# Optimization experiments

Measured on AMD Instinct MI355X. Metric: run time of the kernel, lower is better.

The kernel has to match this reference:

```python
import jax, jax.numpy as jnp
import numpy as np

N_NODES = 50000
N_EDGES = 800000
D_FEAT = 96


def setup_inputs() -> dict:
    key = jax.random.key(0)
    kx, ks, kd = jax.random.split(key, 3)
    x = jax.random.normal(kx, (N_NODES, D_FEAT), dtype=jnp.float32)
    src = jax.random.randint(ks, (N_EDGES,), 0, N_NODES, dtype=jnp.int64)
    dst = jax.random.randint(kd, (N_EDGES,), 0, N_NODES, dtype=jnp.int64)
    return {"x": x, "src": src, "dst": dst}


def reference(x, src, dst):
    n = x.shape[0]
    ones = jnp.ones(src.shape[0], dtype=x.dtype)
    # out-degree: edges leaving each node (src side)
    out_deg = jnp.clip(jax.ops.segment_sum(ones, src, num_segments=n), 1.0, None)
    # in-degree: edges arriving at each node (dst side)
    in_deg = jnp.clip(jax.ops.segment_sum(ones, dst, num_segments=n), 1.0, None)
    # pre-scale by out-degree^{-1/2}
    xs = x * (out_deg ** -0.5)[:, None]
    # copy_u + sum aggregation: sum messages from src into dst
    agg = jax.ops.segment_sum(xs[src], dst, num_segments=n)
    # post-scale by in-degree^{-1/2}
    return agg * (in_deg ** -0.5)[:, None]
```

## Files before the change

### kernel.cpp

```cpp
#include <hip/hip_runtime.h>


#define D_FEAT 96
#define CAP 64
#define PART_SHIFT 8
#define PNODES 256
#define NP_MAX 256
#define EPB 3072
#define OVF_CAP 8192

__device__ __forceinline__ unsigned short f2bf_rne(float f) {
    unsigned u = __float_as_uint(f);
    unsigned r = (u >> 16) & 1u;
    u += 0x7fffu + r;
    return (unsigned short)(u >> 16);
}


__global__ __launch_bounds__(256) void partition_kernel(
        const int* __restrict__ src, const int* __restrict__ dst,
        int n_edges, int np, int stride,
        int* __restrict__ pcur_d, int* __restrict__ pcur_s,
        unsigned* __restrict__ pbuf_d, unsigned short* __restrict__ pbuf_s,
        int* __restrict__ ctr,
        int* __restrict__ povf_d, int* __restrict__ sovf_d) {
    __shared__ int hcd[NP_MAX], hcs[NP_MAX];
    __shared__ int bd[NP_MAX], bs_[NP_MAX];
    __shared__ int od[NP_MAX], os_[NP_MAX];
    const int base = blockIdx.x * EPB;

    for (int i = threadIdx.x; i < NP_MAX; i += 256) {
        hcd[i] = 0; hcs[i] = 0; od[i] = 0; os_[i] = 0;
    }
    __syncthreads();

    unsigned v[12];
    #pragma unroll
    for (int k = 0; k < 12; ++k) {
        int i = base + (int)threadIdx.x + (k << 8);
        if (i < n_edges) {
            int s = src[i], d = dst[i];
            unsigned pv = (unsigned)d | ((unsigned)s << 16);
            v[k] = pv;
            atomicAdd(&hcd[d >> PART_SHIFT], 1);
            atomicAdd(&hcs[s >> PART_SHIFT], 1);
        }
    }
    __syncthreads();

    for (int p = threadIdx.x; p < np; p += 256) {
        int cd = hcd[p];
        bd[p] = cd ? atomicAdd(&pcur_d[p], cd) : 0;
        int cs = hcs[p];
        bs_[p] = cs ? atomicAdd(&pcur_s[p], cs) : 0;
    }
    __syncthreads();

    #pragma unroll
    for (int k = 0; k < 12; ++k) {
        int i = base + (int)threadIdx.x + (k << 8);
        if (i < n_edges) {
            unsigned pv = v[k];
            int d = (int)(pv & 0xffffu);
            int s = (int)(pv >> 16);
            int pd = d >> PART_SHIFT;
            int j = bd[pd] + atomicAdd(&od[pd], 1);
            if (j < stride) pbuf_d[(size_t)pd * stride + j] = pv;
            else { int k2 = atomicAdd(&ctr[1], 1); if (k2 < OVF_CAP) povf_d[k2] = (int)pv; }
            int ps = s >> PART_SHIFT;
            int j2 = bs_[ps] + atomicAdd(&os_[ps], 1);
            if (j2 < stride) pbuf_s[(size_t)ps * stride + j2] = (unsigned short)s;
            else { int k3 = atomicAdd(&ctr[2], 1); if (k3 < OVF_CAP) sovf_d[k3] = s; }
        }
    }
}


__global__ __launch_bounds__(256) void bincnt_kernel(
        const unsigned* __restrict__ pbuf_d, const int* __restrict__ pcur_d,
        const unsigned short* __restrict__ pbuf_s, const int* __restrict__ pcur_s,
        int stride, int n_nodes,
        const float* __restrict__ x, unsigned* __restrict__ xs,
        int* __restrict__ cursor, int* __restrict__ out_cnt,
        unsigned short* __restrict__ slots,
        int* __restrict__ ctr, int* __restrict__ ovf_d) {
    __shared__ unsigned short lslots[PNODES * CAP];
    __shared__ int lcnt[PNODES];
    __shared__ int lout[PNODES];
    const int b = blockIdx.x;
    const int nbase = b << PART_SHIFT;
    const int nloc = min(PNODES, n_nodes - nbase);

    for (int i = threadIdx.x; i < PNODES; i += 256) { lcnt[i] = 0; lout[i] = 0; }
    __syncthreads();

    int n = pcur_d[b]; if (n > stride) n = stride;
    for (int i = threadIdx.x; i < n; i += 256) {
        unsigned pv = pbuf_d[(size_t)b * stride + i];
        int dl = (int)(pv & 0xffu);
        int s  = (int)(pv >> 16);
        int pos = atomicAdd(&lcnt[dl], 1);
        if (pos < CAP) lslots[dl * CAP + pos] = (unsigned short)s;
        else { int k = atomicAdd(&ctr[0], 1); if (k < OVF_CAP) ovf_d[k] = (int)pv; }
    }
    int n2 = pcur_s[b]; if (n2 > stride) n2 = stride;
    for (int i = threadIdx.x; i < n2; i += 256) {
        int s = (int)pbuf_s[(size_t)b * stride + i];
        atomicAdd(&lout[s & (PNODES - 1)], 1);
    }
    __syncthreads();

    for (int i = threadIdx.x; i < nloc; i += 256) {
        cursor[nbase + i]  = lcnt[i];
        out_cnt[nbase + i] = lout[i];
    }
    const unsigned* ls = (const unsigned*)lslots;
    unsigned* gs = (unsigned*)slots + (size_t)nbase * (CAP / 2);
    const int ncopy = nloc * (CAP / 2);
    for (int i = threadIdx.x; i < ncopy; i += 256) gs[i] = ls[i];

    const int ntot = nloc * 48;
    for (int i = threadIdx.x; i < ntot; i += 256) {
        int nd = i / 48;
        int j  = i - nd * 48;
        int c  = lout[nd];
        float w = rsqrtf((float)(c < 1 ? 1 : c));
        float2 vv = *(const float2*)(x + (size_t)(nbase + nd) * D_FEAT + j * 2);
        unsigned lo = f2bf_rne(vv.x * w);
        unsigned hi = f2bf_rne(vv.y * w);
        xs[(size_t)(nbase + nd) * 48 + j] = lo | (hi << 16);
    }
}

__global__ void fixup_kernel(int* __restrict__ ctr,
                             const int* __restrict__ povf_d,
                             const int* __restrict__ sovf_d,
                             int* __restrict__ ovf_d,
                             int* __restrict__ cursor,
                             int* __restrict__ out_cnt,
                             const float* __restrict__ x,
                             unsigned* __restrict__ xs) {
    int np_ = ctr[1]; if (np_ > OVF_CAP) np_ = OVF_CAP;
    for (int i = threadIdx.x; i < np_; i += 256) {
        unsigned pv = (unsigned)povf_d[i];
        atomicAdd(&cursor[pv & 0xffffu], 1);
        int k = atomicAdd(&ctr[0], 1);
        if (k < OVF_CAP) ovf_d[k] = (int)pv;
    }
    int ns_ = ctr[2]; if (ns_ > OVF_CAP) ns_ = OVF_CAP;
    for (int i = threadIdx.x; i < ns_; i += 256)
        atomicAdd(&out_cnt[(unsigned)sovf_d[i]], 1);
    __syncthreads();
    int total = ns_ * 48;
    for (int i = threadIdx.x; i < total; i += 256) {
        int k = i / 48, j = i - k * 48;
        int s = sovf_d[k];
        int c = out_cnt[s];
        float w = rsqrtf((float)(c < 1 ? 1 : c));
        float2 vv = *(const float2*)(x + (size_t)s * D_FEAT + j * 2);
        unsigned lo = f2bf_rne(vv.x * w);
        unsigned hi = f2bf_rne(vv.y * w);
        xs[(size_t)s * 48 + j] = lo | (hi << 16);
    }
}


__global__ __launch_bounds__(256) void gather_kernel(
        const unsigned* __restrict__ xs,
        const unsigned short* __restrict__ slots,
        const int* __restrict__ cursor,
        const float* __restrict__ x,
        const int* __restrict__ out_cnt,
        const int* __restrict__ ctr,
        const int* __restrict__ ovf_d,
        float* __restrict__ out, int n_nodes) {
    int wid  = threadIdx.x >> 6;
    int lane = threadIdx.x & 63;
    int node = __builtin_amdgcn_readfirstlane(blockIdx.x * 4 + wid);
    if (node >= n_nodes) return;

    int cnt_all = __builtin_amdgcn_readfirstlane(cursor[node]);
    int cnt = cnt_all < CAP ? cnt_all : CAP;

    float accx = 0.f, accy = 0.f;
    const bool act = lane < 48;

    if (cnt > 0) {
        int idx  = lane < cnt ? lane : cnt - 1;
        int sval = (int)slots[node * CAP + idx];

        int e = 0;
        for (; e + 16 <= cnt; e += 16) {
            if (act) {
                unsigned u[16];
                #pragma unroll
                for (int k = 0; k < 16; ++k) {
                    int s = __builtin_amdgcn_readlane(sval, e + k);
                    u[k] = xs[s * 48 + lane];
                }
                #pragma unroll
                for (int k = 0; k < 16; ++k) {
                    accx += __uint_as_float(u[k] << 16);
                    accy += __uint_as_float(u[k] & 0xffff0000u);
                }
            }
        }
        for (; e + 4 <= cnt; e += 4) {
            if (act) {
                unsigned u[4];
                #pragma unroll
                for (int k = 0; k < 4; ++k) {
                    int s = __builtin_amdgcn_readlane(sval, e + k);
                    u[k] = xs[s * 48 + lane];
                }
                #pragma unroll
                for (int k = 0; k < 4; ++k) {
                    accx += __uint_as_float(u[k] << 16);
                    accy += __uint_as_float(u[k] & 0xffff0000u);
                }
            }
        }
        for (; e < cnt; ++e) {
            if (act) {
                int s = __builtin_amdgcn_readlane(sval, e);
                unsigned u0 = xs[s * 48 + lane];
                accx += __uint_as_float(u0 << 16);
                accy += __uint_as_float(u0 & 0xffff0000u);
            }
        }
    }

    if (cnt_all > CAP) {
        int novf = __builtin_amdgcn_readfirstlane(ctr[0]);
        if (novf > OVF_CAP) novf = OVF_CAP;
        for (int k = 0; k < novf; ++k) {
            unsigned pv = (unsigned)ovf_d[k];
            if ((int)(pv & 0xffffu) == node) {
                int s = (int)(pv >> 16);
                int c = out_cnt[s];
                float w = rsqrtf((float)(c < 1 ? 1 : c));
                if (act) {
                    accx += w * x[(size_t)s * D_FEAT + lane * 2];
                    accy += w * x[(size_t)s * D_FEAT + lane * 2 + 1];
                }
            }
        }
    }

    float sc = rsqrtf((float)(cnt_all < 1 ? 1 : cnt_all));
    if (act) {
        float* op = out + (size_t)node * D_FEAT + lane * 2;
        op[0] = accx * sc;
        op[1] = accy * sc;
    }
}


__global__ void degree_kernel(const int* __restrict__ src,
                              const int* __restrict__ dst,
                              int* __restrict__ out_cnt,
                              int* __restrict__ in_cnt, int n_edges) {
    int i = blockIdx.x * blockDim.x + threadIdx.x;
    if (i < n_edges) {
        atomicAdd(&out_cnt[src[i]], 1);
        atomicAdd(&in_cnt[dst[i]], 1);
    }
}

__global__ void scale_kernel(float* __restrict__ osc, float* __restrict__ isc, int n) {
    int i = blockIdx.x * blockDim.x + threadIdx.x;
    if (i < n) {
        int c0 = ((const int*)osc)[i];
        int c1 = ((const int*)isc)[i];
        osc[i] = rsqrtf((float)(c0 < 1 ? 1 : c0));
        isc[i] = rsqrtf((float)(c1 < 1 ? 1 : c1));
    }
}

__global__ void scatter_kernel(const float* __restrict__ x,
                               const int* __restrict__ src,
                               const int* __restrict__ dst,
                               const float* __restrict__ osc,
                               const float* __restrict__ isc,
                               float* __restrict__ out, int n_edges) {
    int idx = blockIdx.x * blockDim.x + threadIdx.x;
    int e = idx / 24, c = idx % 24;
    if (e >= n_edges) return;
    int s = src[e], d = dst[e];
    float w = osc[s] * isc[d];
    const float4 v = *(const float4*)(x + (size_t)s * D_FEAT + c * 4);
    float* o = out + (size_t)d * D_FEAT + c * 4;
    unsafeAtomicAdd(o + 0, v.x * w);
    unsafeAtomicAdd(o + 1, v.y * w);
    unsafeAtomicAdd(o + 2, v.z * w);
    unsafeAtomicAdd(o + 3, v.w * w);
}


extern "C" void kernel_launch(void* const* d_in, const int* in_sizes, int n_in,
                              void* d_out, int out_size, void* d_ws, size_t ws_size,
                              hipStream_t stream) {
    const float* x  = (const float*)d_in[0];
    const int* src  = (const int*)d_in[1];
    const int* dst  = (const int*)d_in[2];
    float* out      = (float*)d_out;

    const int n_edges = in_sizes[1];
    const int n_nodes = in_sizes[0] / D_FEAT;

    const int np = (n_nodes + PNODES - 1) / PNODES;
    const int avg = n_edges / (np > 0 ? np : 1);
    const int stride = avg + avg / 4 + 1024;

    const size_t pbuf_words  = (size_t)np * stride;
    const size_t pbufs_words = (pbuf_words + 1) / 2;

    int* pcur_d  = (int*)d_ws;
    int* pcur_s  = pcur_d + 256;
    int* ctr     = pcur_d + 512;
    int* ovf_d   = pcur_d + 1024;
    int* povf_d  = ovf_d + OVF_CAP;
    int* sovf_d  = povf_d + OVF_CAP;
    int* out_cnt = sovf_d + OVF_CAP;
    int* cursor  = out_cnt + 65536;
    unsigned* pbuf_dst = (unsigned*)(cursor + 65536);
    unsigned short* pbuf_src = (unsigned short*)(pbuf_dst + pbuf_words);
    unsigned* xs = pbuf_dst + pbuf_words + pbufs_words;
    unsigned short* slots = (unsigned short*)(xs + (size_t)n_nodes * 48);

    const size_t needed = ((size_t)1024 + 3 * OVF_CAP + 2 * 65536 + pbuf_words +
                           pbufs_words + (size_t)n_nodes * 48 +
                           (size_t)n_nodes * (CAP / 2)) * 4;

    if (ws_size >= needed && n_nodes <= 65536 && np <= NP_MAX) {
        (void)hipMemsetAsync(d_ws, 0, 1024 * sizeof(int), stream);

        partition_kernel<<<(n_edges + EPB - 1) / EPB, 256, 0, stream>>>(
            src, dst, n_edges, np, stride, pcur_d, pcur_s,
            pbuf_dst, pbuf_src, ctr, povf_d, sovf_d);

        bincnt_kernel<<<np, 256, 0, stream>>>(
            pbuf_dst, pcur_d, pbuf_src, pcur_s, stride, n_nodes,
            x, xs, cursor, out_cnt, slots, ctr, ovf_d);

        fixup_kernel<<<1, 256, 0, stream>>>(
            ctr, povf_d, sovf_d, ovf_d, cursor, out_cnt, x, xs);

        gather_kernel<<<(n_nodes + 3) / 4, 256, 0, stream>>>(
            xs, slots, cursor, x, out_cnt, ctr, ovf_d, out, n_nodes);
    } else {
        float* osc = (float*)d_ws;
        float* isc = osc + 65536;
        (void)hipMemsetAsync(d_ws, 0, 2 * 65536 * sizeof(int), stream);
        (void)hipMemsetAsync(d_out, 0, (size_t)out_size * sizeof(float), stream);
        degree_kernel<<<(n_edges + 255) / 256, 256, 0, stream>>>(
            src, dst, (int*)osc, (int*)isc, n_edges);
        scale_kernel<<<(n_nodes + 255) / 256, 256, 0, stream>>>(osc, isc, n_nodes);
        const int total = n_edges * 24;
        scatter_kernel<<<(total + 255) / 256, 256, 0, stream>>>(
            x, src, dst, osc, isc, out, n_edges);
    }
}
```

Measured before the change: 149.7 us.

## Count out-degree with global atomics instead of partitioning source indices

Out-degree counting moves from a second partitioned buffer of source indices, later histogrammed in bincnt, to direct global atomicAdd on out_cnt during partitioning. This drops the pbuf_src writes and reads, the source overflow path and its fixup work, and the memset now clears the out_cnt array. Edges per partition block also rise from 3072 to 4096. The cost is 800k scattered global atomics on a 50k-entry array, which may contend, in exchange for less buffer traffic.

```diff
diff --git a/kernel.cpp b/kernel.cpp
--- a/kernel.cpp
+++ b/kernel.cpp
@@ -6,7 +6,7 @@
 #define PART_SHIFT 8
 #define PNODES 256
 #define NP_MAX 256
-#define EPB 3072
+#define EPB 4096
 #define OVF_CAP 8192
 
 __device__ __forceinline__ unsigned short f2bf_rne(float f) {
@@ -20,30 +20,28 @@
 __global__ __launch_bounds__(256) void partition_kernel(
         const int* __restrict__ src, const int* __restrict__ dst,
         int n_edges, int np, int stride,
-        int* __restrict__ pcur_d, int* __restrict__ pcur_s,
-        unsigned* __restrict__ pbuf_d, unsigned short* __restrict__ pbuf_s,
+        int* __restrict__ pcur_d, int* __restrict__ out_cnt,
+        unsigned* __restrict__ pbuf_d,
         int* __restrict__ ctr,
-        int* __restrict__ povf_d, int* __restrict__ sovf_d) {
-    __shared__ int hcd[NP_MAX], hcs[NP_MAX];
-    __shared__ int bd[NP_MAX], bs_[NP_MAX];
-    __shared__ int od[NP_MAX], os_[NP_MAX];
+        int* __restrict__ povf_d) {
+    __shared__ int hcd[NP_MAX];
+    __shared__ int bd[NP_MAX];
+    __shared__ int od[NP_MAX];
     const int base = blockIdx.x * EPB;
 
-    for (int i = threadIdx.x; i < NP_MAX; i += 256) {
-        hcd[i] = 0; hcs[i] = 0; od[i] = 0; os_[i] = 0;
-    }
-    __syncthreads();
-
-    unsigned v[12];
+    for (int i = threadIdx.x; i < NP_MAX; i += 256) { hcd[i] = 0; od[i] = 0; }
+    __syncthreads();
+
+    unsigned v[16];
     #pragma unroll
-    for (int k = 0; k < 12; ++k) {
+    for (int k = 0; k < 16; ++k) {
         int i = base + (int)threadIdx.x + (k << 8);
         if (i < n_edges) {
             int s = src[i], d = dst[i];
             unsigned pv = (unsigned)d | ((unsigned)s << 16);
             v[k] = pv;
             atomicAdd(&hcd[d >> PART_SHIFT], 1);
-            atomicAdd(&hcs[s >> PART_SHIFT], 1);
+            atomicAdd(&out_cnt[s], 1);
         }
     }
     __syncthreads();
@@ -51,26 +49,19 @@
     for (int p = threadIdx.x; p < np; p += 256) {
         int cd = hcd[p];
         bd[p] = cd ? atomicAdd(&pcur_d[p], cd) : 0;
-        int cs = hcs[p];
-        bs_[p] = cs ? atomicAdd(&pcur_s[p], cs) : 0;
     }
     __syncthreads();
 
     #pragma unroll
-    for (int k = 0; k < 12; ++k) {
+    for (int k = 0; k < 16; ++k) {
         int i = base + (int)threadIdx.x + (k << 8);
         if (i < n_edges) {
             unsigned pv = v[k];
             int d = (int)(pv & 0xffffu);
-            int s = (int)(pv >> 16);
             int pd = d >> PART_SHIFT;
             int j = bd[pd] + atomicAdd(&od[pd], 1);
             if (j < stride) pbuf_d[(size_t)pd * stride + j] = pv;
             else { int k2 = atomicAdd(&ctr[1], 1); if (k2 < OVF_CAP) povf_d[k2] = (int)pv; }
-            int ps = s >> PART_SHIFT;
-            int j2 = bs_[ps] + atomicAdd(&os_[ps], 1);
-            if (j2 < stride) pbuf_s[(size_t)ps * stride + j2] = (unsigned short)s;
-            else { int k3 = atomicAdd(&ctr[2], 1); if (k3 < OVF_CAP) sovf_d[k3] = s; }
         }
     }
 }
@@ -78,10 +69,10 @@
 
 __global__ __launch_bounds__(256) void bincnt_kernel(
         const unsigned* __restrict__ pbuf_d, const int* __restrict__ pcur_d,
-        const unsigned short* __restrict__ pbuf_s, const int* __restrict__ pcur_s,
         int stride, int n_nodes,
         const float* __restrict__ x, unsigned* __restrict__ xs,
-        int* __restrict__ cursor, int* __restrict__ out_cnt,
+        const int* __restrict__ out_cnt,
+        int* __restrict__ cursor,
         unsigned short* __restrict__ slots,
         int* __restrict__ ctr, int* __restrict__ ovf_d) {
     __shared__ unsigned short lslots[PNODES * CAP];
@@ -91,7 +82,8 @@
     const int nbase = b << PART_SHIFT;
     const int nloc = min(PNODES, n_nodes - nbase);
 
-    for (int i = threadIdx.x; i < PNODES; i += 256) { lcnt[i] = 0; lout[i] = 0; }
+    for (int i = threadIdx.x; i < PNODES; i += 256) lcnt[i] = 0;
+    for (int i = threadIdx.x; i < nloc; i += 256) lout[i] = out_cnt[nbase + i];
     __syncthreads();
 
     int n = pcur_d[b]; if (n > stride) n = stride;
@@ -103,17 +95,9 @@
         if (pos < CAP) lslots[dl * CAP + pos] = (unsigned short)s;
         else { int k = atomicAdd(&ctr[0], 1); if (k < OVF_CAP) ovf_d[k] = (int)pv; }
     }
-    int n2 = pcur_s[b]; if (n2 > stride) n2 = stride;
-    for (int i = threadIdx.x; i < n2; i += 256) {
-        int s = (int)pbuf_s[(size_t)b * stride + i];
-        atomicAdd(&lout[s & (PNODES - 1)], 1);
-    }
-    __syncthreads();
-
-    for (int i = threadIdx.x; i < nloc; i += 256) {
-        cursor[nbase + i]  = lcnt[i];
-        out_cnt[nbase + i] = lout[i];
-    }
+    __syncthreads();
+
+    for (int i = threadIdx.x; i < nloc; i += 256) cursor[nbase + i] = lcnt[i];
     const unsigned* ls = (const unsigned*)lslots;
     unsigned* gs = (unsigned*)slots + (size_t)nbase * (CAP / 2);
     const int ncopy = nloc * (CAP / 2);
@@ -134,33 +118,14 @@
 
 __global__ void fixup_kernel(int* __restrict__ ctr,
                              const int* __restrict__ povf_d,
-                             const int* __restrict__ sovf_d,
                              int* __restrict__ ovf_d,
-                             int* __restrict__ cursor,
-                             int* __restrict__ out_cnt,
-                             const float* __restrict__ x,
-                             unsigned* __restrict__ xs) {
+                             int* __restrict__ cursor) {
     int np_ = ctr[1]; if (np_ > OVF_CAP) np_ = OVF_CAP;
     for (int i = threadIdx.x; i < np_; i += 256) {
         unsigned pv = (unsigned)povf_d[i];
         atomicAdd(&cursor[pv & 0xffffu], 1);
         int k = atomicAdd(&ctr[0], 1);
         if (k < OVF_CAP) ovf_d[k] = (int)pv;
-    }
-    int ns_ = ctr[2]; if (ns_ > OVF_CAP) ns_ = OVF_CAP;
-    for (int i = threadIdx.x; i < ns_; i += 256)
-        atomicAdd(&out_cnt[(unsigned)sovf_d[i]], 1);
-    __syncthreads();
-    int total = ns_ * 48;
-    for (int i = threadIdx.x; i < total; i += 256) {
-        int k = i / 48, j = i - k * 48;
-        int s = sovf_d[k];
-        int c = out_cnt[s];
-        float w = rsqrtf((float)(c < 1 ? 1 : c));
-        float2 vv = *(const float2*)(x + (size_t)s * D_FEAT + j * 2);
-        unsigned lo = f2bf_rne(vv.x * w);
-        unsigned hi = f2bf_rne(vv.y * w);
-        xs[(size_t)s * 48 + j] = lo | (hi << 16);
     }
 }
 
@@ -312,39 +277,33 @@
     const int avg = n_edges / (np > 0 ? np : 1);
     const int stride = avg + avg / 4 + 1024;
 
-    const size_t pbuf_words  = (size_t)np * stride;
-    const size_t pbufs_words = (pbuf_words + 1) / 2;
+    const size_t pbuf_words = (size_t)np * stride;
 
     int* pcur_d  = (int*)d_ws;
-    int* pcur_s  = pcur_d + 256;
-    int* ctr     = pcur_d + 512;
-    int* ovf_d   = pcur_d + 1024;
+    int* ctr     = pcur_d + 256;
+    int* out_cnt = pcur_d + 512;
+    int* ovf_d   = out_cnt + 65536;
     int* povf_d  = ovf_d + OVF_CAP;
-    int* sovf_d  = povf_d + OVF_CAP;
-    int* out_cnt = sovf_d + OVF_CAP;
-    int* cursor  = out_cnt + 65536;
+    int* cursor  = povf_d + OVF_CAP;
     unsigned* pbuf_dst = (unsigned*)(cursor + 65536);
-    unsigned short* pbuf_src = (unsigned short*)(pbuf_dst + pbuf_words);
-    unsigned* xs = pbuf_dst + pbuf_words + pbufs_words;
+    unsigned* xs = pbuf_dst + pbuf_words;
     unsigned short* slots = (unsigned short*)(xs + (size_t)n_nodes * 48);
 
-    const size_t needed = ((size_t)1024 + 3 * OVF_CAP + 2 * 65536 + pbuf_words +
-                           pbufs_words + (size_t)n_nodes * 48 +
-                           (size_t)n_nodes * (CAP / 2)) * 4;
+    const size_t needed = ((size_t)512 + 2 * 65536 + 2 * OVF_CAP + pbuf_words +
+                           (size_t)n_nodes * 48 + (size_t)n_nodes * (CAP / 2)) * 4;
 
     if (ws_size >= needed && n_nodes <= 65536 && np <= NP_MAX) {
-        (void)hipMemsetAsync(d_ws, 0, 1024 * sizeof(int), stream);
+        (void)hipMemsetAsync(d_ws, 0, (512 + 65536) * sizeof(int), stream);
 
         partition_kernel<<<(n_edges + EPB - 1) / EPB, 256, 0, stream>>>(
-            src, dst, n_edges, np, stride, pcur_d, pcur_s,
-            pbuf_dst, pbuf_src, ctr, povf_d, sovf_d);
+            src, dst, n_edges, np, stride, pcur_d, out_cnt,
+            pbuf_dst, ctr, povf_d);
 
         bincnt_kernel<<<np, 256, 0, stream>>>(
-            pbuf_dst, pcur_d, pbuf_src, pcur_s, stride, n_nodes,
-            x, xs, cursor, out_cnt, slots, ctr, ovf_d);
-
-        fixup_kernel<<<1, 256, 0, stream>>>(
-            ctr, povf_d, sovf_d, ovf_d, cursor, out_cnt, x, xs);
+            pbuf_dst, pcur_d, stride, n_nodes,
+            x, xs, out_cnt, cursor, slots, ctr, ovf_d);
+
+        fixup_kernel<<<1, 256, 0, stream>>>(ctr, povf_d, ovf_d, cursor);
 
         gather_kernel<<<(n_nodes + 3) / 4, 256, 0, stream>>>(
             xs, slots, cursor, x, out_cnt, ctr, ovf_d, out, n_nodes);
```

New measurement: 165.8 us. 1.11x slower.

## Fold overflow fixup into bincnt, widen xs conversion, retune partition block size

Applied to the files above, without the earlier changes.

Removes the single-block fixup kernel launch: each bincnt block now scans the partition-overflow lists and handles the entries that belong to its own node range before writing counts and scaled features. The bf16 conversion of x now loads float4 and stores uint2 per thread, halving the loop iterations. The partition kernel processes 13 edges per thread (3328 per block) so the grid fits in at most 256 blocks, and a guard on that was added. The cost is that every bincnt block scans the full overflow arrays, which are normally empty.

```diff
diff --git a/kernel.cpp b/kernel.cpp
--- a/kernel.cpp
+++ b/kernel.cpp
@@ -6,7 +6,8 @@
 #define PART_SHIFT 8
 #define PNODES 256
 #define NP_MAX 256
-#define EPB 3072
+#define EPB 3328
+#define EREG 13
 #define OVF_CAP 8192
 
 __device__ __forceinline__ unsigned short f2bf_rne(float f) {
@@ -34,9 +35,9 @@
     }
     __syncthreads();
 
-    unsigned v[12];
+    unsigned v[EREG];
     #pragma unroll
-    for (int k = 0; k < 12; ++k) {
+    for (int k = 0; k < EREG; ++k) {
         int i = base + (int)threadIdx.x + (k << 8);
         if (i < n_edges) {
             int s = src[i], d = dst[i];
@@ -57,7 +58,7 @@
     __syncthreads();
 
     #pragma unroll
-    for (int k = 0; k < 12; ++k) {
+    for (int k = 0; k < EREG; ++k) {
         int i = base + (int)threadIdx.x + (k << 8);
         if (i < n_edges) {
             unsigned pv = v[k];
@@ -83,7 +84,9 @@
         const float* __restrict__ x, unsigned* __restrict__ xs,
         int* __restrict__ cursor, int* __restrict__ out_cnt,
         unsigned short* __restrict__ slots,
-        int* __restrict__ ctr, int* __restrict__ ovf_d) {
+        int* __restrict__ ctr,
+        const int* __restrict__ povf_d, const int* __restrict__ sovf_d,
+        int* __restrict__ ovf_d) {
     __shared__ unsigned short lslots[PNODES * CAP];
     __shared__ int lcnt[PNODES];
     __shared__ int lout[PNODES];
@@ -108,6 +111,28 @@
         int s = (int)pbuf_s[(size_t)b * stride + i];
         atomicAdd(&lout[s & (PNODES - 1)], 1);
     }
+    int npv = ctr[1];
+    if (npv > 0) {
+        if (npv > OVF_CAP) npv = OVF_CAP;
+        for (int i = threadIdx.x; i < npv; i += 256) {
+            unsigned pv = (unsigned)povf_d[i];
+            int d = (int)(pv & 0xffffu);
+            if ((d >> PART_SHIFT) == b) {
+                int dl = d & (PNODES - 1);
+                int pos = atomicAdd(&lcnt[dl], 1);
+                if (pos < CAP) lslots[dl * CAP + pos] = (unsigned short)(pv >> 16);
+                else { int k = atomicAdd(&ctr[0], 1); if (k < OVF_CAP) ovf_d[k] = (int)pv; }
+            }
+        }
+    }
+    int nsv = ctr[2];
+    if (nsv > 0) {
+        if (nsv > OVF_CAP) nsv = OVF_CAP;
+        for (int i = threadIdx.x; i < nsv; i += 256) {
+            int s = sovf_d[i];
+            if ((s >> PART_SHIFT) == b) atomicAdd(&lout[s & (PNODES - 1)], 1);
+        }
+    }
     __syncthreads();
 
     for (int i = threadIdx.x; i < nloc; i += 256) {
@@ -119,48 +144,19 @@
     const int ncopy = nloc * (CAP / 2);
     for (int i = threadIdx.x; i < ncopy; i += 256) gs[i] = ls[i];
 
-    const int ntot = nloc * 48;
+    const int ntot = nloc * 24;
     for (int i = threadIdx.x; i < ntot; i += 256) {
-        int nd = i / 48;
-        int j  = i - nd * 48;
+        int nd = i / 24;
+        int j  = i - nd * 24;
         int c  = lout[nd];
         float w = rsqrtf((float)(c < 1 ? 1 : c));
-        float2 vv = *(const float2*)(x + (size_t)(nbase + nd) * D_FEAT + j * 2);
-        unsigned lo = f2bf_rne(vv.x * w);
-        unsigned hi = f2bf_rne(vv.y * w);
-        xs[(size_t)(nbase + nd) * 48 + j] = lo | (hi << 16);
-    }
-}
-
-__global__ void fixup_kernel(int* __restrict__ ctr,
-                             const int* __restrict__ povf_d,
-                             const int* __restrict__ sovf_d,
-                             int* __restrict__ ovf_d,
-                             int* __restrict__ cursor,
-                             int* __restrict__ out_cnt,
-                             const float* __restrict__ x,
-                             unsigned* __restrict__ xs) {
-    int np_ = ctr[1]; if (np_ > OVF_CAP) np_ = OVF_CAP;
-    for (int i = threadIdx.x; i < np_; i += 256) {
-        unsigned pv = (unsigned)povf_d[i];
-        atomicAdd(&cursor[pv & 0xffffu], 1);
-        int k = atomicAdd(&ctr[0], 1);
-        if (k < OVF_CAP) ovf_d[k] = (int)pv;
-    }
-    int ns_ = ctr[2]; if (ns_ > OVF_CAP) ns_ = OVF_CAP;
-    for (int i = threadIdx.x; i < ns_; i += 256)
-        atomicAdd(&out_cnt[(unsigned)sovf_d[i]], 1);
-    __syncthreads();
-    int total = ns_ * 48;
-    for (int i = threadIdx.x; i < total; i += 256) {
-        int k = i / 48, j = i - k * 48;
-        int s = sovf_d[k];
-        int c = out_cnt[s];
-        float w = rsqrtf((float)(c < 1 ? 1 : c));
-        float2 vv = *(const float2*)(x + (size_t)s * D_FEAT + j * 2);
-        unsigned lo = f2bf_rne(vv.x * w);
-        unsigned hi = f2bf_rne(vv.y * w);
-        xs[(size_t)s * 48 + j] = lo | (hi << 16);
+        float4 vv = ((const float4*)(x + (size_t)(nbase + nd) * D_FEAT))[j];
+        unsigned lo0 = f2bf_rne(vv.x * w), hi0 = f2bf_rne(vv.y * w);
+        unsigned lo1 = f2bf_rne(vv.z * w), hi1 = f2bf_rne(vv.w * w);
+        uint2 o;
+        o.x = lo0 | (hi0 << 16);
+        o.y = lo1 | (hi1 << 16);
+        ((uint2*)(xs + (size_t)(nbase + nd) * 48))[j] = o;
     }
 }
 
@@ -311,6 +307,7 @@
     const int np = (n_nodes + PNODES - 1) / PNODES;
     const int avg = n_edges / (np > 0 ? np : 1);
     const int stride = avg + avg / 4 + 1024;
+    const int pblocks = (n_edges + EPB - 1) / EPB;
 
     const size_t pbuf_words  = (size_t)np * stride;
     const size_t pbufs_words = (pbuf_words + 1) / 2;
@@ -332,19 +329,16 @@
                            pbufs_words + (size_t)n_nodes * 48 +
                            (size_t)n_nodes * (CAP / 2)) * 4;
 
-    if (ws_size >= needed && n_nodes <= 65536 && np <= NP_MAX) {
+    if (ws_size >= needed && n_nodes <= 65536 && np <= NP_MAX && pblocks <= 256) {
         (void)hipMemsetAsync(d_ws, 0, 1024 * sizeof(int), stream);
 
-        partition_kernel<<<(n_edges + EPB - 1) / EPB, 256, 0, stream>>>(
+        partition_kernel<<<pblocks, 256, 0, stream>>>(
             src, dst, n_edges, np, stride, pcur_d, pcur_s,
             pbuf_dst, pbuf_src, ctr, povf_d, sovf_d);
 
         bincnt_kernel<<<np, 256, 0, stream>>>(
             pbuf_dst, pcur_d, pbuf_src, pcur_s, stride, n_nodes,
-            x, xs, cursor, out_cnt, slots, ctr, ovf_d);
-
-        fixup_kernel<<<1, 256, 0, stream>>>(
-            ctr, povf_d, sovf_d, ovf_d, cursor, out_cnt, x, xs);
+            x, xs, cursor, out_cnt, slots, ctr, povf_d, sovf_d, ovf_d);
 
         gather_kernel<<<(n_nodes + 3) / 4, 256, 0, stream>>>(
             xs, slots, cursor, x, out_cnt, ctr, ovf_d, out, n_nodes);
```

New measurement: 138.2 us. 7.7% less time.
